# Performance work log

Measured on AMD Instinct MI355X. Metric: run time of the kernel, lower is better.

The kernel has to match this reference:

```python
import jax, jax.numpy as jnp
import numpy as np

VOCAB, DIM = 100000, 128
B, C, NEG = 4096, 20, 10


def _init_table(key):
    initrange = 0.5 / DIM
    w = jax.random.uniform(key, (VOCAB - 1, DIM), dtype=jnp.float32,
                           minval=-initrange, maxval=initrange)
    return jnp.concatenate([jnp.zeros((1, DIM), jnp.float32), w], axis=0)


def setup_inputs() -> dict:
    key = jax.random.key(0)
    k1, k2, k3, k4, k5 = jax.random.split(key, 5)
    i_words = jax.random.randint(k1, (1, B), 0, VOCAB)
    o_words = jax.random.randint(k2, (C, B), 0, VOCAB)
    n_words = jax.random.randint(k3, (B, C * NEG), 0, VOCAB)
    W_i = _init_table(k4)
    W_os = _init_table(k5)
    return {"i_words": i_words, "o_words": o_words, "n_words": n_words,
            "W_i": W_i, "W_os": W_os}


def reference(i_words, o_words, n_words, W_i, W_os):
    # permute to batch-major
    i_ctx = i_words.T[:, 0]          # [B]  (single center word per example)
    o_ctx = o_words.T                # [B, C]

    i_vec = W_i[i_ctx]               # [B, D]
    o_vec = W_os[o_ctx]              # [B, C, D]
    o_vec_n = -W_os[n_words]         # [B, C*NEG, D]

    # bmm(o_vec, i_vec^T).sum(-1) -> positive scores [B, C]
    pos = jnp.einsum('bcd,bd->bc', o_vec, i_vec)
    loss_pos = jax.nn.log_sigmoid(pos).mean(axis=-1)              # [B]

    # negative scores [B, C*NEG] -> [B, C, NEG] -> mean over NEG
    neg = jnp.einsum('bnd,bd->bn', o_vec_n, i_vec)
    loss_neg = jax.nn.log_sigmoid(neg).reshape(-1, C, NEG).mean(axis=-1)  # [B, C]

    loss = jnp.sum(loss_pos) + jnp.sum(loss_neg)
    return -loss
```

## Files before the change

### kernel.cpp

```cpp
#include <hip/hip_runtime.h>
#include <math.h>

#define VOCAB 100000
#define DIM 128
#define BATCH 4096
#define CTX 20
#define NEGS 10
#define NTARG 220
#define NB 32
#define ROWS_PER_B 3125
#define CAP 16
#define SPILL_PER_BLK 64
#define SPILL_BLOCKS 8

#define OFF_COUNTS    0u
#define OFF_SPILLCNTB 131072u
#define OFF_SPILLB    132096u
#define OFF_RECORDS   197632u
#define OFF_IVEC8     4391936u
#define OFF_WOS8      4916224u
#define WS_NEEDED     17716224u
#define CONV_BLOCKS   3125

#if defined(__has_builtin)
#if __has_builtin(__builtin_amdgcn_sdot4)
#define USE_SDOT4 1
#endif
#endif

#define QSCALE 32512.0f
#define INV_QS2 (1.0f / (32512.0f * 32512.0f))

__device__ __forceinline__ float log_sigmoid_fast(float x) {
    float a = fabsf(x);
    return fminf(x, 0.0f) - __logf(1.0f + __expf(-a));
}

__device__ __forceinline__ int q8(float x) {
    int q = (int)rintf(x * QSCALE);
    return q < -127 ? -127 : (q > 127 ? 127 : q);
}
__device__ __forceinline__ unsigned pack4(float a, float b, float c, float d) {
    return (unsigned)(q8(a) & 255) | ((unsigned)(q8(b) & 255) << 8)
         | ((unsigned)(q8(c) & 255) << 16) | ((unsigned)(q8(d) & 255) << 24);
}

__device__ __forceinline__ int dot4(unsigned a, unsigned b, int c) {
#ifdef USE_SDOT4
    return __builtin_amdgcn_sdot4((int)a, (int)b, c, false);
#else
    #pragma unroll
    for (int k = 0; k < 4; ++k) {
        int av = ((int)(a << (24 - 8 * k))) >> 24;
        int bv = ((int)(b << (24 - 8 * k))) >> 24;
        c += av * bv;
    }
    return c;
#endif
}

__global__ __launch_bounds__(256) void prep_kernel(
    const int* __restrict__ i_words, const int* __restrict__ o_words,
    const int* __restrict__ n_words, const float4* __restrict__ W_i4,
    const float4* __restrict__ W_os4, unsigned* __restrict__ ivec8,
    unsigned* __restrict__ wos8, unsigned short* __restrict__ records,
    unsigned char* __restrict__ counts, unsigned* __restrict__ spillcntb,
    unsigned* __restrict__ spillb, float* __restrict__ out)
{
    if (blockIdx.x >= 384) {
        unsigned tid3 = (blockIdx.x - 384) * 256 + threadIdx.x;
        float4 a = W_os4[tid3 * 4];
        float4 b = W_os4[tid3 * 4 + 1];
        float4 c = W_os4[tid3 * 4 + 2];
        float4 d = W_os4[tid3 * 4 + 3];
        uint4 o;
        o.x = pack4(a.x, a.y, a.z, a.w);
        o.y = pack4(b.x, b.y, b.z, b.w);
        o.z = pack4(c.x, c.y, c.z, c.w);
        o.w = pack4(d.x, d.y, d.z, d.w);
        ((uint4*)wos8)[tid3] = o;
        return;
    }
    if (blockIdx.x >= 256) {
        int gtid = (blockIdx.x - 256) * 256 + threadIdx.x;
        int ex = gtid >> 3, part = gtid & 7;
        const float4* src = W_i4 + (size_t)i_words[ex] * 32 + part * 4;
        float4 a = src[0], b = src[1], c = src[2], d = src[3];
        uint4 o;
        o.x = pack4(a.x, a.y, a.z, a.w);
        o.y = pack4(b.x, b.y, b.z, b.w);
        o.z = pack4(c.x, c.y, c.z, c.w);
        o.w = pack4(d.x, d.y, d.z, d.w);
        ((uint4*)ivec8)[gtid] = o;
        return;
    }
    if (blockIdx.x == 0 && threadIdx.x == 0) out[0] = 0.0f;

    __shared__ unsigned       lcnt[NB * 16];
    __shared__ unsigned short lrec[NB * 16 * CAP];
    __shared__ unsigned       lspill[SPILL_PER_BLK];
    __shared__ unsigned       lspill_cnt;
    const int exl = threadIdx.x >> 4;
    const int tt  = threadIdx.x & 15;
    const int b   = blockIdx.x * 16 + exl;

    for (int k = threadIdx.x; k < NB * 16; k += 256) lcnt[k] = 0;
    if (threadIdx.x == 0) lspill_cnt = 0;
    __syncthreads();

    for (int j = tt; j < NTARG; j += 16) {
        int idx; unsigned negbit;
        if (j < CTX) { idx = o_words[j * BATCH + b];                negbit = 0u; }
        else         { idx = n_words[b * (CTX * NEGS) + (j - CTX)]; negbit = 0x1000u; }
        unsigned bucket = (unsigned)idx / ROWS_PER_B;
        unsigned rl     = (unsigned)idx - bucket * ROWS_PER_B;
        unsigned slot = atomicAdd(&lcnt[bucket * 16 + (unsigned)exl], 1u);
        if (slot < CAP) {
            lrec[(bucket * 16 + (unsigned)exl) * CAP + slot] = (unsigned short)(rl | negbit);
        } else {
            unsigned s = atomicAdd(&lspill_cnt, 1u);
            if (s < SPILL_PER_BLK)
                lspill[s] = ((unsigned)idx << 13) | ((unsigned)b << 1) | (negbit ? 1u : 0u);
        }
    }
    __syncthreads();
    for (int k = threadIdx.x; k < NB * 16; k += 256) {
        unsigned c = lcnt[k];
        unsigned bucket = (unsigned)k >> 4, e2 = (unsigned)k & 15u;
        counts[(bucket << 12) + (unsigned)blockIdx.x * 16 + e2] = (unsigned char)(c < CAP ? c : CAP);
    }
    unsigned sc = lspill_cnt; if (sc > SPILL_PER_BLK) sc = SPILL_PER_BLK;
    if (threadIdx.x == 0) spillcntb[blockIdx.x] = sc;
    for (unsigned k = threadIdx.x; k < sc; k += 256)
        spillb[(unsigned)blockIdx.x * SPILL_PER_BLK + k] = lspill[k];

    const unsigned* lrec32 = (const unsigned*)lrec;
    unsigned* grec32 = (unsigned*)records;
    for (int k = threadIdx.x; k < NB * 128; k += 256) {
        unsigned bucket = (unsigned)k >> 7;
        unsigned within = (unsigned)k & 127u;
        grec32[((bucket << 12) + (unsigned)blockIdx.x * 16u) * 8u + within] = lrec32[k];
    }
}

__global__ __launch_bounds__(256) void bucket_loss_i8_kernel(
    const unsigned* __restrict__ wos8, const unsigned* __restrict__ ivec8,
    const float* __restrict__ W_os, const float* __restrict__ W_i,
    const int* __restrict__ i_words,
    const unsigned short* __restrict__ records, const unsigned char* __restrict__ counts,
    const unsigned* __restrict__ spillcntb, const unsigned* __restrict__ spillb,
    float* __restrict__ out)
{
    const int t    = threadIdx.x & 7;
    const int grp  = threadIdx.x >> 3;
    const int lane = threadIdx.x & 63;
    const int wave = threadIdx.x >> 6;
    const unsigned tb8 = (unsigned)t << 4;
    const unsigned* rec32 = (const unsigned*)records;

    float acc = 0.0f;
    const int lid = blockIdx.x;

    if (lid < 2048) {
        const int xcd  = lid & 7;
        const int s    = lid >> 3;
        const int half = s >> 7;
        const unsigned bcell = ((unsigned)(s & 127)) * 32u + (unsigned)grp;

        const uint4 iv = *(const uint4*)((const char*)ivec8 + ((bcell << 7) + tb8));

        for (int hb = 0; hb < 2; ++hb) {
            const unsigned bucket = (unsigned)(xcd * 4 + half * 2 + hb);
            const unsigned cell   = (bucket << 12) + bcell;
            const unsigned cnt    = counts[cell];
            unsigned w = rec32[cell * 8u + (unsigned)t];

            for (unsigned base = 0; base < cnt; base += 4) {
                unsigned recs[4]; uint4 rw[4];
                #pragma unroll
                for (int i = 0; i < 4; ++i) {
                    unsigned ji = base + (unsigned)i;
                    int src = (grp << 3) + (int)(ji >> 1);
                    unsigned wv  = __shfl(w, src, 64);
                    unsigned rec = (ji & 1u) ? (wv >> 16) : (wv & 0xffffu);
                    recs[i] = rec;
                    unsigned rowg = (ji < cnt) ? (bucket * ROWS_PER_B + (rec & 0xfffu)) : 0u;
                    rw[i] = *(const uint4*)((const char*)wos8 + ((rowg << 7) + tb8));
                }
                #pragma unroll
                for (int i = 0; i < 4; ++i) {
                    unsigned ji = base + (unsigned)i;
                    int id = dot4(rw[i].x, iv.x, 0);
                    id = dot4(rw[i].y, iv.y, id);
                    id = dot4(rw[i].z, iv.z, id);
                    id = dot4(rw[i].w, iv.w, id);
                    float pd = (float)id * INV_QS2;
                    pd += __shfl_xor(pd, 1);
                    pd += __shfl_xor(pd, 2);
                    pd += __shfl_xor(pd, 4);
                    float term = (recs[i] & 0x1000u)
                               ? (1.0f / NEGS) * log_sigmoid_fast(-pd)
                               : (1.0f / CTX)  * log_sigmoid_fast(pd);
                    if (t == 0 && ji < cnt) acc += term;
                }
            }
        }
    } else {
        const int t16   = threadIdx.x & 15;
        const int grp16 = threadIdx.x >> 4;
        const int rb = (lid - 2048) * 32;
        for (int rr = 0; rr < 32; ++rr) {
            unsigned cnt = spillcntb[rb + rr];
            if (cnt > SPILL_PER_BLK) cnt = SPILL_PER_BLK;
            for (unsigned s = grp16; s < cnt; s += 16) {
                unsigned e = spillb[(unsigned)(rb + rr) * SPILL_PER_BLK + s];
                unsigned row = e >> 13, bb = (e >> 1) & 4095u;
                const char* rp = (const char*)W_os + ((row << 9) + ((unsigned)t16 << 5));
                float4 r0 = *(const float4*)rp, r1 = *(const float4*)(rp + 16);
                const char* vp = (const char*)W_i + (((unsigned)i_words[bb] << 9) + ((unsigned)t16 << 5));
                float4 v0 = *(const float4*)vp, v1 = *(const float4*)(vp + 16);
                float pd = r0.x*v0.x + r0.y*v0.y + r0.z*v0.z + r0.w*v0.w
                         + r1.x*v1.x + r1.y*v1.y + r1.z*v1.z + r1.w*v1.w;
                pd += __shfl_xor(pd, 1);
                pd += __shfl_xor(pd, 2);
                pd += __shfl_xor(pd, 4);
                pd += __shfl_xor(pd, 8);
                float term = (e & 1u) ? (1.0f / NEGS) * log_sigmoid_fast(-pd)
                                      : (1.0f / CTX)  * log_sigmoid_fast(pd);
                if (t16 == 0) acc += term;
            }
        }
    }

    acc += __shfl_xor(acc, 8);
    acc += __shfl_xor(acc, 16);
    acc += __shfl_xor(acc, 32);
    __shared__ float wsum[4];
    if (lane == 0) wsum[wave] = acc;
    __syncthreads();
    if (threadIdx.x == 0) {
        float sum = wsum[0] + wsum[1] + wsum[2] + wsum[3];
        if (sum != 0.0f) atomicAdd(out, -sum);
    }
}

__global__ __launch_bounds__(256) void sgns_loss_direct(
    const int* __restrict__ i_words, const int* __restrict__ o_words,
    const int* __restrict__ n_words, const float* __restrict__ W_i,
    const float* __restrict__ W_os, float* __restrict__ out)
{
    const int lane = threadIdx.x & 63;
    const int wave = threadIdx.x >> 6;
    const int w    = blockIdx.x * 4 + wave;
    const int b    = w >> 1;
    const int h    = w & 1;
    const int sub = lane >> 4;
    const int t   = lane & 15;
    const int j_begin = h ? 112 : 0;
    const int j_end   = h ? NTARG : 112;
    float acc = 0.0f;
    const int ic = i_words[b];
    const char* ibase = (const char*)W_i + (((unsigned)ic << 9) + ((unsigned)t << 5));
    float4 i0 = *(const float4*)(ibase);
    float4 i1 = *(const float4*)(ibase + 16);
    #pragma unroll 4
    for (int j0 = j_begin; j0 < j_end; j0 += 4) {
        int jj = j0 + sub;
        int idx; float sgn, wgt;
        if (jj < CTX) { idx = o_words[jj * BATCH + b]; sgn = 1.0f; wgt = 1.0f / CTX; }
        else { idx = n_words[b * (CTX * NEGS) + (jj - CTX)]; sgn = -1.0f; wgt = 1.0f / NEGS; }
        const char* obase = (const char*)W_os + (((unsigned)idx << 9) + ((unsigned)t << 5));
        float4 o0 = *(const float4*)(obase);
        float4 o1 = *(const float4*)(obase + 16);
        float p = i0.x*o0.x + i0.y*o0.y + i0.z*o0.z + i0.w*o0.w
                + i1.x*o1.x + i1.y*o1.y + i1.z*o1.z + i1.w*o1.w;
        p += __shfl_xor(p, 1); p += __shfl_xor(p, 2);
        p += __shfl_xor(p, 4); p += __shfl_xor(p, 8);
        acc += (t == 0) ? wgt * log_sigmoid_fast(sgn * p) : 0.0f;
    }
    acc += __shfl_xor(acc, 16);
    acc += __shfl_xor(acc, 32);
    __shared__ float ws[4];
    if (lane == 0) ws[wave] = acc;
    __syncthreads();
    if (threadIdx.x == 0) atomicAdd(out, -(ws[0] + ws[1] + ws[2] + ws[3]));
}

extern "C" void kernel_launch(void* const* d_in, const int* in_sizes, int n_in,
                              void* d_out, int out_size, void* d_ws, size_t ws_size,
                              hipStream_t stream) {
    const int*   i_words = (const int*)d_in[0];
    const int*   o_words = (const int*)d_in[1];
    const int*   n_words = (const int*)d_in[2];
    const float* W_i     = (const float*)d_in[3];
    const float* W_os    = (const float*)d_in[4];
    float* out = (float*)d_out;

    if (ws_size < (size_t)WS_NEEDED) {
        hipMemsetAsync(out, 0, sizeof(float), stream);
        sgns_loss_direct<<<2048, 256, 0, stream>>>(i_words, o_words, n_words, W_i, W_os, out);
        return;
    }

    char* ws = (char*)d_ws;
    unsigned char*  counts    = (unsigned char*)(ws + OFF_COUNTS);
    unsigned*       spillcntb = (unsigned*)(ws + OFF_SPILLCNTB);
    unsigned*       spillb    = (unsigned*)(ws + OFF_SPILLB);
    unsigned short* records   = (unsigned short*)(ws + OFF_RECORDS);
    unsigned*       ivec8     = (unsigned*)(ws + OFF_IVEC8);
    unsigned*       wos8      = (unsigned*)(ws + OFF_WOS8);

    prep_kernel<<<384 + CONV_BLOCKS, 256, 0, stream>>>(
        i_words, o_words, n_words, (const float4*)W_i, (const float4*)W_os,
        ivec8, wos8, records, counts, spillcntb, spillb, out);
    bucket_loss_i8_kernel<<<2048 + SPILL_BLOCKS, 256, 0, stream>>>(
        wos8, ivec8, W_os, W_i, i_words, records, counts, spillcntb, spillb, out);
}
```

Measured before the change: 62.38 us.

## Stream bucket rows through LDS with double-buffered global_load_lds pipeline

Replaces the unrolled batch of four register row loads in the bucketed int8 loss loop with a per-wave, double-buffered pipeline built on direct global-to-LDS loads. Each iteration waits for the older load, reads the row slice from LDS, and issues the load two records ahead, so fetch latency overlaps the dot products. The loop runs to the wave-wide maximum count, so groups with fewer records do wasted clamped loads. The buffer reuse around the LDS read and the vmcnt-based waits are delicate and could race or stall if the compiler reorders memory operations.

```diff
diff --git a/kernel.cpp b/kernel.cpp
--- a/kernel.cpp
+++ b/kernel.cpp
@@ -25,6 +25,9 @@
 #if defined(__has_builtin)
 #if __has_builtin(__builtin_amdgcn_sdot4)
 #define USE_SDOT4 1
+#endif
+#if __has_builtin(__builtin_amdgcn_global_load_lds)
+#define HAVE_GLLDS 1
 #endif
 #endif
 
@@ -158,6 +161,10 @@
     const unsigned tb8 = (unsigned)t << 4;
     const unsigned* rec32 = (const unsigned*)records;
 
+#ifdef HAVE_GLLDS
+    __shared__ char stage[4][2][1024];
+#endif
+
     float acc = 0.0f;
     const int lid = blockIdx.x;
 
@@ -175,6 +182,58 @@
             const unsigned cnt    = counts[cell];
             unsigned w = rec32[cell * 8u + (unsigned)t];
 
+#ifdef HAVE_GLLDS
+            unsigned wmax = cnt;
+            { int m = (int)wmax, o;
+              o = __shfl_xor(m, 8);  m = m > o ? m : o;
+              o = __shfl_xor(m, 16); m = m > o ? m : o;
+              o = __shfl_xor(m, 32); m = m > o ? m : o;
+              wmax = (unsigned)m; }
+            if (wmax) {
+                const unsigned rowbase = bucket * ROWS_PER_B;
+                char* buf0 = &stage[wave][0][0];
+                char* buf1 = &stage[wave][1][0];
+
+                #define BCAST_REC(J, RECV) { \
+                    unsigned jj_ = (J); \
+                    unsigned jc_ = (jj_ < cnt) ? jj_ : (cnt ? cnt - 1u : 0u); \
+                    unsigned wv_ = __shfl(w, (grp << 3) + (int)(jc_ >> 1), 64); \
+                    RECV = (jc_ & 1u) ? (wv_ >> 16) : (wv_ & 0xffffu); }
+                #define ISSUE_ROW(RECV, BUF) { \
+                    unsigned rowg_ = rowbase + ((RECV) & 0xfffu); \
+                    const char* gp_ = (const char*)wos8 + (((size_t)rowg_) << 7) + tb8; \
+                    __builtin_amdgcn_global_load_lds( \
+                        (const __attribute__((address_space(1))) unsigned*)(const void*)gp_, \
+                        (__attribute__((address_space(3))) unsigned*)(void*)(BUF), 16, 0, 0); }
+
+                asm volatile("s_waitcnt vmcnt(0)" ::: "memory");
+                unsigned rc0, rc1, rc2;
+                BCAST_REC(0u, rc0); ISSUE_ROW(rc0, buf0);
+                BCAST_REC(1u, rc1); ISSUE_ROW(rc1, buf1);
+                for (unsigned j = 0; j < wmax; ++j) {
+                    asm volatile("s_waitcnt vmcnt(1)" ::: "memory");
+                    const char* cur = (j & 1u) ? buf1 : buf0;
+                    uint4 rv = *(const uint4*)(cur + ((unsigned)lane << 4));
+                    BCAST_REC(j + 2u, rc2);
+                    ISSUE_ROW(rc2, ((j & 1u) ? buf1 : buf0));
+                    int id = dot4(rv.x, iv.x, 0);
+                    id = dot4(rv.y, iv.y, id);
+                    id = dot4(rv.z, iv.z, id);
+                    id = dot4(rv.w, iv.w, id);
+                    float pd = (float)id * INV_QS2;
+                    pd += __shfl_xor(pd, 1);
+                    pd += __shfl_xor(pd, 2);
+                    pd += __shfl_xor(pd, 4);
+                    float term = (rc0 & 0x1000u)
+                               ? (1.0f / NEGS) * log_sigmoid_fast(-pd)
+                               : (1.0f / CTX)  * log_sigmoid_fast(pd);
+                    if (t == 0 && j < cnt) acc += term;
+                    rc0 = rc1; rc1 = rc2;
+                }
+                #undef BCAST_REC
+                #undef ISSUE_ROW
+            }
+#else
             for (unsigned base = 0; base < cnt; base += 4) {
                 unsigned recs[4]; uint4 rw[4];
                 #pragma unroll
@@ -204,7 +263,11 @@
                     if (t == 0 && ji < cnt) acc += term;
                 }
             }
+#endif
         }
+#ifdef HAVE_GLLDS
+        asm volatile("s_waitcnt vmcnt(0)" ::: "memory");
+#endif
     } else {
         const int t16   = threadIdx.x & 15;
         const int grp16 = threadIdx.x >> 4;
```

Measured after the change: 66.65 us. +6.9%, slower.
